# Kernel optimization log

Hardware: AMD Instinct MI355X
Metric: run time of the kernel (lower is better)

Reference implementation:

```python
import jax, jax.numpy as jnp
import numpy as np

B, T, D, E, H = 4, 1024, 1024, 8, 2048


def setup_inputs() -> dict:
    key = jax.random.key(0)
    ks = jax.random.split(key, 5)
    # Kaiming-uniform-ish init scales (exact values irrelevant for correctness baseline)
    bound_bank = 1.0 / np.sqrt(D)
    bound_down = 1.0 / np.sqrt(H)
    return {
        "x": jax.random.normal(ks[0], (B, T, D), dtype=jnp.float32),
        "gate_w": jax.random.uniform(ks[1], (E, D), jnp.float32, -bound_bank, bound_bank),
        "gate_bank": jax.random.uniform(ks[2], (E, D, H), jnp.float32, -bound_bank, bound_bank),
        "up_bank": jax.random.uniform(ks[3], (E, D, H), jnp.float32, -bound_bank, bound_bank),
        "down_bank": jax.random.uniform(ks[4], (E, H, D), jnp.float32, -bound_down, bound_down),
    }


def reference(x, gate_w, gate_bank, up_bank, down_bank):
    # Router logits: [B,T,E] (nn.Linear with weight [E,D], no bias)
    logits = jnp.einsum('btd,ed->bte', x, gate_w)
    selected = jnp.argmax(logits, axis=-1)          # [B,T] int
    # Dense all-expert SwiGLU
    u = jnp.einsum('btd,edh->bteh', x, up_bank)     # [B,T,E,H]
    a = jnp.einsum('btd,edh->bteh', x, gate_bank)   # [B,T,E,H]
    h = jax.nn.silu(a) * u                          # [B,T,E,H]
    y = jnp.einsum('bteh,ehd->bted', h, down_bank)  # [B,T,E,D]
    # Gather argmax-selected expert output per token
    idx = selected[:, :, None, None]                # [B,T,1,1]
    out = jnp.take_along_axis(y, idx, axis=2)[:, :, 0, :]  # [B,T,D]
    return out
```

## Files before the change

### kernel.cpp

```cpp
#include <hip/hip_runtime.h>
#include <hip/hip_bf16.h>

#define NTOK 4096
#define DDIM 1024
#define HDIM 2048
#define NEXP 8

typedef __attribute__((ext_vector_type(4))) float f32x4;
typedef __attribute__((ext_vector_type(8))) short bf16x8;
typedef __attribute__((ext_vector_type(8))) unsigned short us8;

__device__ __forceinline__ unsigned short f2bf(float f) {
    unsigned u = __float_as_uint(f);
    unsigned r = (u + 0x7fffu + ((u >> 16) & 1u)) >> 16;
    return (unsigned short)r;
}

__global__ void gate_kernel(const float* __restrict__ x, const float* __restrict__ gw,
                            int* __restrict__ sel) {
    int t = blockIdx.x;
    int tid = threadIdx.x, lane = tid & 63, w = tid >> 6;
    __shared__ double red[NEXP];
    const float* xr = x + (size_t)t * DDIM;
    #pragma unroll
    for (int s = 0; s < 2; ++s) {
        int e = w * 2 + s;
        const float* g = gw + (size_t)e * DDIM;
        double acc = 0.0;
        #pragma unroll
        for (int j = 0; j < DDIM / 64; ++j) {
            int d = lane + j * 64;
            acc += (double)xr[d] * (double)g[d];
        }
        #pragma unroll
        for (int off = 32; off; off >>= 1) acc += __shfl_down(acc, off);
        if (lane == 0) red[e] = acc;
    }
    __syncthreads();
    if (tid == 0) {
        int best = 0; double bv = red[0];
        #pragma unroll
        for (int e = 1; e < NEXP; ++e) if (red[e] > bv) { bv = red[e]; best = e; }
        sel[t] = best;
    }
}

__global__ void scatter_kernel(const int* __restrict__ sel, int* __restrict__ cnt,
                               int* __restrict__ perm) {
    int t = blockIdx.x * blockDim.x + threadIdx.x;
    if (t < NTOK) {
        int e = sel[t];
        int p = atomicAdd(&cnt[e], 1);
        perm[e * NTOK + p] = t;
    }
}

__global__ __launch_bounds__(256) void stage_a(
        const float* __restrict__ x, const float* __restrict__ gb,
        const float* __restrict__ ub, const int* __restrict__ cnt,
        const int* __restrict__ perm, unsigned short* __restrict__ hws) {
    const int e = blockIdx.z;
    const int n0 = blockIdx.x * 64;
    const int m0 = blockIdx.y * 64;
    const int count = cnt[e];
    if (m0 >= count) return;
    const int* pl = perm + e * NTOK;

    __shared__ unsigned short Xs[64 * 64];
    __shared__ unsigned short Gt[64 * 64];
    __shared__ unsigned short Ut[64 * 64];

    const int tid = threadIdx.x;
    const int lane = tid & 63, w = tid >> 6;
    const int wr = w >> 1, wc = w & 1;
    const int lg = lane >> 4, li = lane & 15;

    f32x4 accG[2][2] = {{{0.f,0.f,0.f,0.f},{0.f,0.f,0.f,0.f}},{{0.f,0.f,0.f,0.f},{0.f,0.f,0.f,0.f}}};
    f32x4 accU[2][2] = {{{0.f,0.f,0.f,0.f},{0.f,0.f,0.f,0.f}},{{0.f,0.f,0.f,0.f},{0.f,0.f,0.f,0.f}}};

    const int xr = tid >> 2;
    int tok_x = -1;
    if (m0 + xr < count) tok_x = pl[m0 + xr];
    const int kstage = tid >> 2;

    for (int k0 = 0; k0 < DDIM; k0 += 64) {
        __syncthreads();
        {
            #pragma unroll
            for (int j = 0; j < 4; ++j) {
                int f4 = (tid & 3) + 4 * j;
                ushort4 v = {0, 0, 0, 0};
                if (tok_x >= 0) {
                    const float4 g = *reinterpret_cast<const float4*>(
                        x + (size_t)tok_x * DDIM + k0 + f4 * 4);
                    v.x = f2bf(g.x); v.y = f2bf(g.y); v.z = f2bf(g.z); v.w = f2bf(g.w);
                }
                int blk = f4 >> 1;
                int sb = blk ^ (xr & 7);
                *reinterpret_cast<ushort4*>(Xs + xr * 64 + sb * 8 + (f4 & 1) * 4) = v;
            }
        }
        {
            const float* gRow = gb + ((size_t)e * DDIM + k0 + kstage) * HDIM + n0;
            const float* uRow = ub + ((size_t)e * DDIM + k0 + kstage) * HDIM + n0;
            const int kb = kstage >> 3, ki = kstage & 7;
            #pragma unroll
            for (int j = 0; j < 4; ++j) {
                int f4 = (tid & 3) + 4 * j;
                float4 gv = *reinterpret_cast<const float4*>(gRow + f4 * 4);
                float4 uv = *reinterpret_cast<const float4*>(uRow + f4 * 4);
                #pragma unroll
                for (int c = 0; c < 4; ++c) {
                    int n = f4 * 4 + c;
                    int idx = n * 64 + ((kb ^ (n & 7)) << 3) + ki;
                    Gt[idx] = f2bf(((const float*)&gv)[c]);
                    Ut[idx] = f2bf(((const float*)&uv)[c]);
                }
            }
        }
        __syncthreads();
        #pragma unroll
        for (int kf = 0; kf < 2; ++kf) {
            const int kb = kf * 4 + lg;
            bf16x8 af[2], bg[2], bu[2];
            #pragma unroll
            for (int mi = 0; mi < 2; ++mi) {
                int r = wr * 32 + mi * 16 + li;
                af[mi] = *reinterpret_cast<const bf16x8*>(Xs + r * 64 + ((kb ^ (r & 7)) << 3));
            }
            #pragma unroll
            for (int ni = 0; ni < 2; ++ni) {
                int n = wc * 32 + ni * 16 + li;
                int off = n * 64 + ((kb ^ (n & 7)) << 3);
                bg[ni] = *reinterpret_cast<const bf16x8*>(Gt + off);
                bu[ni] = *reinterpret_cast<const bf16x8*>(Ut + off);
            }
            #pragma unroll
            for (int mi = 0; mi < 2; ++mi)
                #pragma unroll
                for (int ni = 0; ni < 2; ++ni) {
                    accG[mi][ni] = __builtin_amdgcn_mfma_f32_16x16x32_bf16(af[mi], bg[ni], accG[mi][ni], 0, 0, 0);
                    accU[mi][ni] = __builtin_amdgcn_mfma_f32_16x16x32_bf16(af[mi], bu[ni], accU[mi][ni], 0, 0, 0);
                }
        }
    }
    #pragma unroll
    for (int mi = 0; mi < 2; ++mi) {
        #pragma unroll
        for (int r = 0; r < 4; ++r) {
            int row = m0 + wr * 32 + mi * 16 + lg * 4 + r;
            if (row < count) {
                int tok = pl[row];
                #pragma unroll
                for (int ni = 0; ni < 2; ++ni) {
                    float a = accG[mi][ni][r];
                    float u = accU[mi][ni][r];
                    float h = (a / (1.0f + __expf(-a))) * u;
                    hws[(size_t)tok * HDIM + n0 + wc * 32 + ni * 16 + li] = f2bf(h);
                }
            }
        }
    }
}

__global__ __launch_bounds__(256) void stage_b(
        const unsigned short* __restrict__ hws, const float* __restrict__ db,
        const int* __restrict__ cnt, const int* __restrict__ perm,
        float* __restrict__ out) {
    const int e = blockIdx.z;
    const int d0 = blockIdx.x * 64;
    const int m0 = blockIdx.y * 64;
    const int count = cnt[e];
    if (m0 >= count) return;
    const int* pl = perm + e * NTOK;

    __shared__ unsigned short Hs[64 * 64];
    __shared__ unsigned short Dt[64 * 64];

    const int tid = threadIdx.x;
    const int lane = tid & 63, w = tid >> 6;
    const int wr = w >> 1, wc = w & 1;
    const int lg = lane >> 4, li = lane & 15;

    f32x4 acc[2][2] = {{{0.f,0.f,0.f,0.f},{0.f,0.f,0.f,0.f}},{{0.f,0.f,0.f,0.f},{0.f,0.f,0.f,0.f}}};

    const int xr = tid >> 2;
    int tok_x = -1;
    if (m0 + xr < count) tok_x = pl[m0 + xr];
    const int kstage = tid >> 2;

    for (int k0 = 0; k0 < HDIM; k0 += 64) {
        __syncthreads();
        {
            #pragma unroll
            for (int j = 0; j < 2; ++j) {
                int blk = (tid & 3) + 4 * j;
                us8 v = {0,0,0,0,0,0,0,0};
                if (tok_x >= 0)
                    v = *reinterpret_cast<const us8*>(hws + (size_t)tok_x * HDIM + k0 + blk * 8);
                int sb = blk ^ (xr & 7);
                *reinterpret_cast<us8*>(Hs + xr * 64 + sb * 8) = v;
            }
        }
        {
            const float* dRow = db + ((size_t)e * HDIM + k0 + kstage) * DDIM + d0;
            const int kb = kstage >> 3, ki = kstage & 7;
            #pragma unroll
            for (int j = 0; j < 4; ++j) {
                int f4 = (tid & 3) + 4 * j;
                float4 dv = *reinterpret_cast<const float4*>(dRow + f4 * 4);
                #pragma unroll
                for (int c = 0; c < 4; ++c) {
                    int n = f4 * 4 + c;
                    int idx = n * 64 + ((kb ^ (n & 7)) << 3) + ki;
                    Dt[idx] = f2bf(((const float*)&dv)[c]);
                }
            }
        }
        __syncthreads();
        #pragma unroll
        for (int kf = 0; kf < 2; ++kf) {
            const int kb = kf * 4 + lg;
            bf16x8 af[2], bd[2];
            #pragma unroll
            for (int mi = 0; mi < 2; ++mi) {
                int r = wr * 32 + mi * 16 + li;
                af[mi] = *reinterpret_cast<const bf16x8*>(Hs + r * 64 + ((kb ^ (r & 7)) << 3));
            }
            #pragma unroll
            for (int ni = 0; ni < 2; ++ni) {
                int n = wc * 32 + ni * 16 + li;
                bd[ni] = *reinterpret_cast<const bf16x8*>(Dt + n * 64 + ((kb ^ (n & 7)) << 3));
            }
            #pragma unroll
            for (int mi = 0; mi < 2; ++mi)
                #pragma unroll
                for (int ni = 0; ni < 2; ++ni)
                    acc[mi][ni] = __builtin_amdgcn_mfma_f32_16x16x32_bf16(af[mi], bd[ni], acc[mi][ni], 0, 0, 0);
        }
    }
    #pragma unroll
    for (int mi = 0; mi < 2; ++mi) {
        #pragma unroll
        for (int r = 0; r < 4; ++r) {
            int row = m0 + wr * 32 + mi * 16 + lg * 4 + r;
            if (row < count) {
                int tok = pl[row];
                #pragma unroll
                for (int ni = 0; ni < 2; ++ni)
                    out[(size_t)tok * DDIM + d0 + wc * 32 + ni * 16 + li] = acc[mi][ni][r];
            }
        }
    }
}

extern "C" void kernel_launch(void* const* d_in, const int* in_sizes, int n_in,
                              void* d_out, int out_size, void* d_ws, size_t ws_size,
                              hipStream_t stream) {
    const float* x  = (const float*)d_in[0];
    const float* gw = (const float*)d_in[1];
    const float* gb = (const float*)d_in[2];
    const float* ub = (const float*)d_in[3];
    const float* db = (const float*)d_in[4];
    float* out = (float*)d_out;

    char* ws = (char*)d_ws;
    int* cnt = (int*)(ws);
    int* sel = (int*)(ws + 256);
    int* perm = (int*)(ws + 256 + 16384);
    unsigned short* hws = (unsigned short*)(ws + 256 + 16384 + 131072);

    hipMemsetAsync(cnt, 0, 256, stream);
    gate_kernel<<<NTOK, 256, 0, stream>>>(x, gw, sel);
    scatter_kernel<<<NTOK / 256, 256, 0, stream>>>(sel, cnt, perm);
    stage_a<<<dim3(HDIM / 64, NTOK / 64, NEXP), 256, 0, stream>>>(x, gb, ub, cnt, perm, hws);
    stage_b<<<dim3(DDIM / 64, NTOK / 64, NEXP), 256, 0, stream>>>(hws, db, cnt, perm, out);
}
```

Baseline: 403.5 us.

## Pre-cast weights to transposed bf16 and use 128x128 direct-to-LDS GEMM tiles

Adds separate cast kernels that convert x and all weight banks to bf16, with gate/up transposed and interleaved into one K-major bank and down transposed. The expert GEMMs then use 128x128 tiles fed by global_load_lds 16-byte async copies into swizzled LDS, which removes per-tile float conversion and scattered LDS writes. Gate and up become one fused N=4096 GEMM whose interleaved column pairs feed the SwiGLU epilogue. The cost is an extra full pass over every weight bank on each call (all experts, including ones with few tokens) and a larger workspace.

```diff
diff --git a/kernel.cpp b/kernel.cpp
--- a/kernel.cpp
+++ b/kernel.cpp
@@ -12,8 +12,48 @@
 
 __device__ __forceinline__ unsigned short f2bf(float f) {
     unsigned u = __float_as_uint(f);
-    unsigned r = (u + 0x7fffu + ((u >> 16) & 1u)) >> 16;
-    return (unsigned short)r;
+    return (unsigned short)((u + 0x7fffu + ((u >> 16) & 1u)) >> 16);
+}
+
+__device__ __forceinline__ void gload16(const void* g, void* l) {
+    __builtin_amdgcn_global_load_lds((const __attribute__((address_space(1))) void*)g,
+                                     (__attribute__((address_space(3))) void*)l, 16, 0, 0);
+}
+
+__global__ void xcast(const float* __restrict__ x, unsigned short* __restrict__ xb) {
+    int i = blockIdx.x * blockDim.x + threadIdx.x;
+    float4 v = reinterpret_cast<const float4*>(x)[i];
+    ushort4 o = { f2bf(v.x), f2bf(v.y), f2bf(v.z), f2bf(v.w) };
+    reinterpret_cast<ushort4*>(xb)[i] = o;
+}
+
+__global__ __launch_bounds__(256) void tcast(const float* __restrict__ src,
+        unsigned short* __restrict__ dst, int R, int C, int interleave, int upoff,
+        long long estride) {
+    __shared__ unsigned short __attribute__((aligned(16))) tile[64][80];
+    const int e = blockIdx.z, r0 = blockIdx.y * 64, c0 = blockIdx.x * 64;
+    const float* s = src + ((size_t)e * R + r0) * C + c0;
+    const int t = threadIdx.x;
+    const int rd = t >> 2;
+    #pragma unroll
+    for (int j = 0; j < 4; ++j) {
+        int c4 = (t & 3) * 4 + j;
+        float4 v = *reinterpret_cast<const float4*>(s + (size_t)rd * C + c4 * 4);
+        tile[c4 * 4 + 0][rd] = f2bf(v.x);
+        tile[c4 * 4 + 1][rd] = f2bf(v.y);
+        tile[c4 * 4 + 2][rd] = f2bf(v.z);
+        tile[c4 * 4 + 3][rd] = f2bf(v.w);
+    }
+    __syncthreads();
+    const int cr = t >> 2;
+    const int c = c0 + cr;
+    const int orow = interleave ? (((c >> 4) << 5) + (c & 15) + upoff) : c;
+    unsigned short* drow = dst + (size_t)e * estride + (size_t)orow * R + r0;
+    #pragma unroll
+    for (int j = 0; j < 2; ++j) {
+        int ch = (t & 3) + j * 4;
+        *reinterpret_cast<us8*>(drow + ch * 8) = *reinterpret_cast<const us8*>(&tile[cr][ch * 8]);
+    }
 }
 
 __global__ void gate_kernel(const float* __restrict__ x, const float* __restrict__ gw,
@@ -56,107 +96,84 @@
 }
 
 __global__ __launch_bounds__(256) void stage_a(
-        const float* __restrict__ x, const float* __restrict__ gb,
-        const float* __restrict__ ub, const int* __restrict__ cnt,
-        const int* __restrict__ perm, unsigned short* __restrict__ hws) {
+        const unsigned short* __restrict__ xb, const unsigned short* __restrict__ wa,
+        const int* __restrict__ cnt, const int* __restrict__ perm,
+        unsigned short* __restrict__ hws) {
     const int e = blockIdx.z;
-    const int n0 = blockIdx.x * 64;
-    const int m0 = blockIdx.y * 64;
+    const int n0 = blockIdx.x * 128;
+    const int m0 = blockIdx.y * 128;
     const int count = cnt[e];
     if (m0 >= count) return;
     const int* pl = perm + e * NTOK;
 
-    __shared__ unsigned short Xs[64 * 64];
-    __shared__ unsigned short Gt[64 * 64];
-    __shared__ unsigned short Ut[64 * 64];
-
-    const int tid = threadIdx.x;
-    const int lane = tid & 63, w = tid >> 6;
-    const int wr = w >> 1, wc = w & 1;
-    const int lg = lane >> 4, li = lane & 15;
-
-    f32x4 accG[2][2] = {{{0.f,0.f,0.f,0.f},{0.f,0.f,0.f,0.f}},{{0.f,0.f,0.f,0.f},{0.f,0.f,0.f,0.f}}};
-    f32x4 accU[2][2] = {{{0.f,0.f,0.f,0.f},{0.f,0.f,0.f,0.f}},{{0.f,0.f,0.f,0.f},{0.f,0.f,0.f,0.f}}};
-
-    const int xr = tid >> 2;
-    int tok_x = -1;
-    if (m0 + xr < count) tok_x = pl[m0 + xr];
-    const int kstage = tid >> 2;
+    __shared__ unsigned short __attribute__((aligned(16))) As[128 * 64];
+    __shared__ unsigned short __attribute__((aligned(16))) Bs[128 * 64];
+
+    const int tid = threadIdx.x, lane = tid & 63, w = tid >> 6;
+    const int wr = w >> 1, wc = w & 1, li = lane & 15, lg = lane >> 4;
+    const int sb = lane & 7, r8 = lane >> 3;
+    const int srcswz = (sb ^ r8) * 8;
+
+    const unsigned short* pA[4];
+    const unsigned short* pB[4];
+    #pragma unroll
+    for (int i = 0; i < 4; ++i) {
+        int row = i * 32 + w * 8 + r8;
+        int tr = m0 + row; if (tr >= count) tr = count - 1;
+        int tok = pl[tr];
+        pA[i] = xb + (size_t)tok * DDIM + srcswz;
+        pB[i] = wa + ((size_t)e * (2 * HDIM) + (size_t)(n0 + row)) * DDIM + srcswz;
+    }
+
+    f32x4 acc[4][4];
+    #pragma unroll
+    for (int i = 0; i < 4; ++i)
+        #pragma unroll
+        for (int j = 0; j < 4; ++j) acc[i][j] = (f32x4){0.f, 0.f, 0.f, 0.f};
 
     for (int k0 = 0; k0 < DDIM; k0 += 64) {
-        __syncthreads();
-        {
-            #pragma unroll
-            for (int j = 0; j < 4; ++j) {
-                int f4 = (tid & 3) + 4 * j;
-                ushort4 v = {0, 0, 0, 0};
-                if (tok_x >= 0) {
-                    const float4 g = *reinterpret_cast<const float4*>(
-                        x + (size_t)tok_x * DDIM + k0 + f4 * 4);
-                    v.x = f2bf(g.x); v.y = f2bf(g.y); v.z = f2bf(g.z); v.w = f2bf(g.w);
-                }
-                int blk = f4 >> 1;
-                int sb = blk ^ (xr & 7);
-                *reinterpret_cast<ushort4*>(Xs + xr * 64 + sb * 8 + (f4 & 1) * 4) = v;
-            }
-        }
-        {
-            const float* gRow = gb + ((size_t)e * DDIM + k0 + kstage) * HDIM + n0;
-            const float* uRow = ub + ((size_t)e * DDIM + k0 + kstage) * HDIM + n0;
-            const int kb = kstage >> 3, ki = kstage & 7;
-            #pragma unroll
-            for (int j = 0; j < 4; ++j) {
-                int f4 = (tid & 3) + 4 * j;
-                float4 gv = *reinterpret_cast<const float4*>(gRow + f4 * 4);
-                float4 uv = *reinterpret_cast<const float4*>(uRow + f4 * 4);
-                #pragma unroll
-                for (int c = 0; c < 4; ++c) {
-                    int n = f4 * 4 + c;
-                    int idx = n * 64 + ((kb ^ (n & 7)) << 3) + ki;
-                    Gt[idx] = f2bf(((const float*)&gv)[c]);
-                    Ut[idx] = f2bf(((const float*)&uv)[c]);
-                }
-            }
-        }
+        #pragma unroll
+        for (int i = 0; i < 4; ++i) gload16(pA[i] + k0, As + (i * 256 + w * 64) * 8);
+        #pragma unroll
+        for (int i = 0; i < 4; ++i) gload16(pB[i] + k0, Bs + (i * 256 + w * 64) * 8);
+        asm volatile("s_waitcnt vmcnt(0)" ::: "memory");
         __syncthreads();
         #pragma unroll
         for (int kf = 0; kf < 2; ++kf) {
+            bf16x8 a[4], b[4];
             const int kb = kf * 4 + lg;
-            bf16x8 af[2], bg[2], bu[2];
-            #pragma unroll
-            for (int mi = 0; mi < 2; ++mi) {
-                int r = wr * 32 + mi * 16 + li;
-                af[mi] = *reinterpret_cast<const bf16x8*>(Xs + r * 64 + ((kb ^ (r & 7)) << 3));
-            }
-            #pragma unroll
-            for (int ni = 0; ni < 2; ++ni) {
-                int n = wc * 32 + ni * 16 + li;
-                int off = n * 64 + ((kb ^ (n & 7)) << 3);
-                bg[ni] = *reinterpret_cast<const bf16x8*>(Gt + off);
-                bu[ni] = *reinterpret_cast<const bf16x8*>(Ut + off);
-            }
-            #pragma unroll
-            for (int mi = 0; mi < 2; ++mi)
-                #pragma unroll
-                for (int ni = 0; ni < 2; ++ni) {
-                    accG[mi][ni] = __builtin_amdgcn_mfma_f32_16x16x32_bf16(af[mi], bg[ni], accG[mi][ni], 0, 0, 0);
-                    accU[mi][ni] = __builtin_amdgcn_mfma_f32_16x16x32_bf16(af[mi], bu[ni], accU[mi][ni], 0, 0, 0);
-                }
-        }
-    }
-    #pragma unroll
-    for (int mi = 0; mi < 2; ++mi) {
+            #pragma unroll
+            for (int mi = 0; mi < 4; ++mi) {
+                int r = wr * 64 + mi * 16 + li;
+                a[mi] = *reinterpret_cast<const bf16x8*>(As + r * 64 + ((kb ^ (li & 7)) << 3));
+            }
+            #pragma unroll
+            for (int ni = 0; ni < 4; ++ni) {
+                int n = wc * 64 + ni * 16 + li;
+                b[ni] = *reinterpret_cast<const bf16x8*>(Bs + n * 64 + ((kb ^ (li & 7)) << 3));
+            }
+            #pragma unroll
+            for (int mi = 0; mi < 4; ++mi)
+                #pragma unroll
+                for (int ni = 0; ni < 4; ++ni)
+                    acc[mi][ni] = __builtin_amdgcn_mfma_f32_16x16x32_bf16(a[mi], b[ni], acc[mi][ni], 0, 0, 0);
+        }
+        __syncthreads();
+    }
+    const int hbase = (n0 >> 1) + wc * 32 + li;
+    #pragma unroll
+    for (int mi = 0; mi < 4; ++mi) {
         #pragma unroll
         for (int r = 0; r < 4; ++r) {
-            int row = m0 + wr * 32 + mi * 16 + lg * 4 + r;
+            int row = m0 + wr * 64 + mi * 16 + lg * 4 + r;
             if (row < count) {
                 int tok = pl[row];
                 #pragma unroll
-                for (int ni = 0; ni < 2; ++ni) {
-                    float a = accG[mi][ni][r];
-                    float u = accU[mi][ni][r];
-                    float h = (a / (1.0f + __expf(-a))) * u;
-                    hws[(size_t)tok * HDIM + n0 + wc * 32 + ni * 16 + li] = f2bf(h);
+                for (int p = 0; p < 2; ++p) {
+                    float a = acc[mi][p * 2 + 0][r];
+                    float u = acc[mi][p * 2 + 1][r];
+                    float h = (a / (1.f + __expf(-a))) * u;
+                    hws[(size_t)tok * HDIM + hbase + p * 16] = f2bf(h);
                 }
             }
         }
@@ -164,91 +181,80 @@
 }
 
 __global__ __launch_bounds__(256) void stage_b(
-        const unsigned short* __restrict__ hws, const float* __restrict__ db,
+        const unsigned short* __restrict__ hws, const unsigned short* __restrict__ wb,
         const int* __restrict__ cnt, const int* __restrict__ perm,
         float* __restrict__ out) {
     const int e = blockIdx.z;
-    const int d0 = blockIdx.x * 64;
-    const int m0 = blockIdx.y * 64;
+    const int n0 = blockIdx.x * 128;
+    const int m0 = blockIdx.y * 128;
     const int count = cnt[e];
     if (m0 >= count) return;
     const int* pl = perm + e * NTOK;
 
-    __shared__ unsigned short Hs[64 * 64];
-    __shared__ unsigned short Dt[64 * 64];
-
-    const int tid = threadIdx.x;
-    const int lane = tid & 63, w = tid >> 6;
-    const int wr = w >> 1, wc = w & 1;
-    const int lg = lane >> 4, li = lane & 15;
-
-    f32x4 acc[2][2] = {{{0.f,0.f,0.f,0.f},{0.f,0.f,0.f,0.f}},{{0.f,0.f,0.f,0.f},{0.f,0.f,0.f,0.f}}};
-
-    const int xr = tid >> 2;
-    int tok_x = -1;
-    if (m0 + xr < count) tok_x = pl[m0 + xr];
-    const int kstage = tid >> 2;
+    __shared__ unsigned short __attribute__((aligned(16))) As[128 * 64];
+    __shared__ unsigned short __attribute__((aligned(16))) Bs[128 * 64];
+
+    const int tid = threadIdx.x, lane = tid & 63, w = tid >> 6;
+    const int wr = w >> 1, wc = w & 1, li = lane & 15, lg = lane >> 4;
+    const int sb = lane & 7, r8 = lane >> 3;
+    const int srcswz = (sb ^ r8) * 8;
+
+    const unsigned short* pA[4];
+    const unsigned short* pB[4];
+    #pragma unroll
+    for (int i = 0; i < 4; ++i) {
+        int row = i * 32 + w * 8 + r8;
+        int tr = m0 + row; if (tr >= count) tr = count - 1;
+        int tok = pl[tr];
+        pA[i] = hws + (size_t)tok * HDIM + srcswz;
+        pB[i] = wb + ((size_t)e * DDIM + (size_t)(n0 + row)) * HDIM + srcswz;
+    }
+
+    f32x4 acc[4][4];
+    #pragma unroll
+    for (int i = 0; i < 4; ++i)
+        #pragma unroll
+        for (int j = 0; j < 4; ++j) acc[i][j] = (f32x4){0.f, 0.f, 0.f, 0.f};
 
     for (int k0 = 0; k0 < HDIM; k0 += 64) {
-        __syncthreads();
-        {
-            #pragma unroll
-            for (int j = 0; j < 2; ++j) {
-                int blk = (tid & 3) + 4 * j;
-                us8 v = {0,0,0,0,0,0,0,0};
-                if (tok_x >= 0)
-                    v = *reinterpret_cast<const us8*>(hws + (size_t)tok_x * HDIM + k0 + blk * 8);
-                int sb = blk ^ (xr & 7);
-                *reinterpret_cast<us8*>(Hs + xr * 64 + sb * 8) = v;
-            }
-        }
-        {
-            const float* dRow = db + ((size_t)e * HDIM + k0 + kstage) * DDIM + d0;
-            const int kb = kstage >> 3, ki = kstage & 7;
-            #pragma unroll
-            for (int j = 0; j < 4; ++j) {
-                int f4 = (tid & 3) + 4 * j;
-                float4 dv = *reinterpret_cast<const float4*>(dRow + f4 * 4);
-                #pragma unroll
-                for (int c = 0; c < 4; ++c) {
-                    int n = f4 * 4 + c;
-                    int idx = n * 64 + ((kb ^ (n & 7)) << 3) + ki;
-                    Dt[idx] = f2bf(((const float*)&dv)[c]);
-                }
-            }
-        }
+        #pragma unroll
+        for (int i = 0; i < 4; ++i) gload16(pA[i] + k0, As + (i * 256 + w * 64) * 8);
+        #pragma unroll
+        for (int i = 0; i < 4; ++i) gload16(pB[i] + k0, Bs + (i * 256 + w * 64) * 8);
+        asm volatile("s_waitcnt vmcnt(0)" ::: "memory");
         __syncthreads();
         #pragma unroll
         for (int kf = 0; kf < 2; ++kf) {
+            bf16x8 a[4], b[4];
             const int kb = kf * 4 + lg;
-            bf16x8 af[2], bd[2];
-            #pragma unroll
-            for (int mi = 0; mi < 2; ++mi) {
-                int r = wr * 32 + mi * 16 + li;
-                af[mi] = *reinterpret_cast<const bf16x8*>(Hs + r * 64 + ((kb ^ (r & 7)) << 3));
-            }
-            #pragma unroll
-            for (int ni = 0; ni < 2; ++ni) {
-                int n = wc * 32 + ni * 16 + li;
-                bd[ni] = *reinterpret_cast<const bf16x8*>(Dt + n * 64 + ((kb ^ (n & 7)) << 3));
-            }
-            #pragma unroll
-            for (int mi = 0; mi < 2; ++mi)
-                #pragma unroll
-                for (int ni = 0; ni < 2; ++ni)
-                    acc[mi][ni] = __builtin_amdgcn_mfma_f32_16x16x32_bf16(af[mi], bd[ni], acc[mi][ni], 0, 0, 0);
-        }
-    }
-    #pragma unroll
-    for (int mi = 0; mi < 2; ++mi) {
+            #pragma unroll
+            for (int mi = 0; mi < 4; ++mi) {
+                int r = wr * 64 + mi * 16 + li;
+                a[mi] = *reinterpret_cast<const bf16x8*>(As + r * 64 + ((kb ^ (li & 7)) << 3));
+            }
+            #pragma unroll
+            for (int ni = 0; ni < 4; ++ni) {
+                int n = wc * 64 + ni * 16 + li;
+                b[ni] = *reinterpret_cast<const bf16x8*>(Bs + n * 64 + ((kb ^ (li & 7)) << 3));
+            }
+            #pragma unroll
+            for (int mi = 0; mi < 4; ++mi)
+                #pragma unroll
+                for (int ni = 0; ni < 4; ++ni)
+                    acc[mi][ni] = __builtin_amdgcn_mfma_f32_16x16x32_bf16(a[mi], b[ni], acc[mi][ni], 0, 0, 0);
+        }
+        __syncthreads();
+    }
+    #pragma unroll
+    for (int mi = 0; mi < 4; ++mi) {
         #pragma unroll
         for (int r = 0; r < 4; ++r) {
-            int row = m0 + wr * 32 + mi * 16 + lg * 4 + r;
+            int row = m0 + wr * 64 + mi * 16 + lg * 4 + r;
             if (row < count) {
                 int tok = pl[row];
                 #pragma unroll
-                for (int ni = 0; ni < 2; ++ni)
-                    out[(size_t)tok * DDIM + d0 + wc * 32 + ni * 16 + li] = acc[mi][ni][r];
+                for (int ni = 0; ni < 4; ++ni)
+                    out[(size_t)tok * DDIM + n0 + wc * 64 + ni * 16 + li] = acc[mi][ni][r];
             }
         }
     }
@@ -265,14 +271,26 @@
     float* out = (float*)d_out;
 
     char* ws = (char*)d_ws;
-    int* cnt = (int*)(ws);
-    int* sel = (int*)(ws + 256);
-    int* perm = (int*)(ws + 256 + 16384);
-    unsigned short* hws = (unsigned short*)(ws + 256 + 16384 + 131072);
+    unsigned short* wbank = (unsigned short*)(ws);
+    unsigned short* hws   = (unsigned short*)(ws + 67108864);
+    unsigned short* xbf   = (unsigned short*)(ws + 67108864 + 16777216);
+    char* misc = ws + 67108864 + 16777216 + 8388608;
+    int* cnt  = (int*)(misc);
+    int* sel  = (int*)(misc + 256);
+    int* perm = (int*)(misc + 256 + 16384);
 
     hipMemsetAsync(cnt, 0, 256, stream);
+    xcast<<<NTOK * DDIM / 4 / 256, 256, 0, stream>>>(x, xbf);
+    tcast<<<dim3(HDIM / 64, DDIM / 64, NEXP), 256, 0, stream>>>(
+        gb, wbank, DDIM, HDIM, 1, 0, (long long)2 * HDIM * DDIM);
+    tcast<<<dim3(HDIM / 64, DDIM / 64, NEXP), 256, 0, stream>>>(
+        ub, wbank, DDIM, HDIM, 1, 16, (long long)2 * HDIM * DDIM);
     gate_kernel<<<NTOK, 256, 0, stream>>>(x, gw, sel);
     scatter_kernel<<<NTOK / 256, 256, 0, stream>>>(sel, cnt, perm);
-    stage_a<<<dim3(HDIM / 64, NTOK / 64, NEXP), 256, 0, stream>>>(x, gb, ub, cnt, perm, hws);
-    stage_b<<<dim3(DDIM / 64, NTOK / 64, NEXP), 256, 0, stream>>>(hws, db, cnt, perm, out);
-}
+    stage_a<<<dim3(2 * HDIM / 128, NTOK / 128, NEXP), 256, 0, stream>>>(
+        xbf, wbank, cnt, perm, hws);
+    tcast<<<dim3(DDIM / 64, HDIM / 64, NEXP), 256, 0, stream>>>(
+        db, wbank, HDIM, DDIM, 0, 0, (long long)DDIM * HDIM);
+    stage_b<<<dim3(DDIM / 128, NTOK / 128, NEXP), 256, 0, stream>>>(
+        hws, wbank, cnt, perm, out);
+}
```

Measured after the change: 372.0 us. 1.08x faster.
